# Optimization experiments

Hardware: AMD Instinct MI355X
Metric: run time of the kernel (lower is better)

## Reference

```python
import jax, jax.numpy as jnp
import numpy as np

B, N, D, K = 4, 8192, 128, 16


def setup_inputs() -> dict:
    key = jax.random.key(0)
    ks = jax.random.split(key, 12)
    w = lambda k, s: (jax.random.normal(k, s, jnp.float32) * 0.02)
    return {
        "xyz": jax.random.normal(ks[0], (B, N, 3), jnp.float32),
        "feat": jax.random.normal(ks[1], (B, N, D), jnp.float32),
        # Linear weights stored as (in, out); apply as x @ W + b
        "Wq": w(ks[2], (D, D)), "bq": jnp.zeros((D,), jnp.float32),
        "Wk": w(ks[3], (D, D)), "bk": jnp.zeros((D,), jnp.float32),
        "Wv": w(ks[4], (D, D)), "bv": jnp.zeros((D,), jnp.float32),
        "Wp1": w(ks[5], (3, D)), "bp1": jnp.zeros((D,), jnp.float32),
        "Wp2": w(ks[6], (D, D)), "bp2": jnp.zeros((D,), jnp.float32),
        "Wo": w(ks[7], (D, D)), "bo": jnp.zeros((D,), jnp.float32),
        "gamma": jnp.float32(0.5),
    }


def reference(xyz, feat, Wq, bq, Wk, bk, Wv, bv, Wp1, bp1, Wp2, bp2, Wo, bo, gamma):
    # pairwise squared distance (B,N,N)
    sq = jnp.sum(xyz * xyz, axis=-1)
    dist = sq[:, :, None] + sq[:, None, :] - 2.0 * jnp.einsum("bnc,bmc->bnm", xyz, xyz)
    # K nearest neighbors (smallest distance)
    _, idx = jax.lax.top_k(-dist, K)  # (B,N,K)
    bidx = jnp.arange(B)[:, None, None]
    n_xyz = xyz[bidx, idx]    # (B,N,K,3)
    n_feat = feat[bidx, idx]  # (B,N,K,D)

    q = (feat @ Wq + bq)[:, :, None, :]    # (B,N,1,D)
    kk = n_feat @ Wk + bk                  # (B,N,K,D)
    v = n_feat @ Wv + bv                   # (B,N,K,D)

    rel_pos = xyz[:, :, None, :] - n_xyz   # (B,N,K,3)
    pos_enc = jax.nn.relu(rel_pos @ Wp1 + bp1) @ Wp2 + bp2  # (B,N,K,D)

    # per-channel-summed attention score, softmax over neighbor axis
    score = jnp.sum(q - kk + pos_enc, axis=-1, keepdims=True)  # (B,N,K,1)
    attn = jax.nn.softmax(score, axis=-2)

    agg = jnp.sum(attn * (v + pos_enc), axis=2)  # (B,N,D)
    out = agg @ Wo + bo
    return feat + gamma * out
```

## Files before the change

### kernel.cpp

```cpp
#include <hip/hip_runtime.h>
#include <hip/hip_bf16.h>

#define BATCH 4
#define NPTS  8192
#define DIM   128
#define KNN   16
#define NROWS (BATCH * NPTS)

#define SPLITS 16
#define RANGE  512
#define TILE   256
#define DEPTH  32
#define DEPTHP 34
#define NSUB   8

using u64  = unsigned long long;
using u32  = unsigned int;

__device__ __forceinline__ unsigned short f2bf(float f) {
    u32 u = __float_as_uint(f);
    u32 r = (u + 0x7FFFu + ((u >> 16) & 1u)) >> 16;
    return (unsigned short)r;
}
__device__ __forceinline__ u32 fordkey(float f) {
    u32 u = __float_as_uint(f);
    return (u & 0x80000000u) ? ~u : (u | 0x80000000u);
}
__device__ __forceinline__ float invkey(u32 k) {
    u32 u = (k & 0x80000000u) ? (k & 0x7FFFFFFFu) : ~k;
    return __uint_as_float(u);
}

__device__ __forceinline__ void insert16(u64 key, u64* ks) {
    if (key < ks[15]) {
#pragma unroll
        for (int t = 0; t < 16; ++t) {
            u64 lo = key < ks[t] ? key : ks[t];
            u64 hi = key < ks[t] ? ks[t] : key;
            ks[t] = lo;
            key = hi;
        }
    }
}

__device__ __forceinline__ float pdist(float4 me, float4 c) {
    float dot = __fadd_rn(__fadd_rn(__fmul_rn(me.x, c.x), __fmul_rn(me.y, c.y)),
                          __fmul_rn(me.z, c.z));
    return __fsub_rn(__fadd_rn(me.w, c.w), __fmul_rn(2.0f, dot));
}

__global__ __launch_bounds__(256) void prep_weights(const float* __restrict__ Wk,
                                                    const float* __restrict__ Wp2,
                                                    float* __restrict__ wk,
                                                    float* __restrict__ w2) {
    int tid = threadIdx.x;
    int c = tid & 127;
    const float* src = (tid < 128) ? Wk : Wp2;
    float s = 0.f;
    for (int d = 0; d < DIM; ++d) s += src[c * DIM + d];
    if (tid < 128) wk[c] = s;
    else           w2[c] = s;
}

__global__ __launch_bounds__(256) void conv_weights(const float* __restrict__ Wv,
                                                    const float* __restrict__ Wp2,
                                                    const float* __restrict__ Wo,
                                                    u32* __restrict__ Wb) {
    int i = blockIdx.x * 256 + threadIdx.x;
    int which = i >> 13, off = i & 8191;
    const float* W = (which == 0) ? Wv : (which == 1 ? Wp2 : Wo);
    float2 w = ((const float2*)W)[off];
    Wb[i] = (u32)f2bf(w.x) | ((u32)f2bf(w.y) << 16);
}

__global__ __launch_bounds__(256) void prep_points(const float* __restrict__ xyz,
                                                   const float* __restrict__ feat,
                                                   const float* __restrict__ wk,
                                                   float4* __restrict__ pts,
                                                   float* __restrict__ sK) {
    int lid = threadIdx.x & 63;
    int p = blockIdx.x * 4 + (threadIdx.x >> 6);
    float f_lo = feat[(size_t)p * DIM + lid];
    float f_hi = feat[(size_t)p * DIM + 64 + lid];
    float s = fmaf(f_lo, wk[lid], f_hi * wk[64 + lid]);
#pragma unroll
    for (int m = 32; m >= 1; m >>= 1) s += __shfl_xor(s, m);
    if (lid == 0) {
        float x = xyz[p * 3 + 0];
        float y = xyz[p * 3 + 1];
        float z = xyz[p * 3 + 2];
        float sq = __fadd_rn(__fadd_rn(__fmul_rn(x, x), __fmul_rn(y, y)), __fmul_rn(z, z));
        pts[p] = make_float4(x, y, z, sq);
        sK[p] = s;
    }
}

__global__ __launch_bounds__(256) void knn_limpass(const float4* __restrict__ pts,
                                                   float* __restrict__ dlim) {
    __shared__ float4 tile[256];
    __shared__ unsigned short stk[4][64][DEPTHP];
    int y = blockIdx.y;
    int wavein = threadIdx.x >> 6, lane = threadIdx.x & 63;
    int q = blockIdx.x * 256 + wavein * 64 + lane;
    int b = q >> 13;
    float4 me = pts[q];
    {
        float4 c = pts[b * NPTS + y * 256 + threadIdx.x];
        tile[threadIdx.x] = make_float4(c.x, c.y, c.z, -0.5f * c.w);
    }
    __syncthreads();
    float ks[16];
#pragma unroll
    for (int t = 0; t < 16; ++t) ks[t] = INFINITY;
    unsigned short* mystk = stk[wavein][lane];

    for (int jj = 0; jj < 32; ++jj) {
        float4 c = tile[jj];
        float s = fmaf(me.x, c.x, fmaf(me.y, c.y, fmaf(me.z, c.z, c.w)));
        float d = fmaf(-2.0f, s, me.w);
        if (d < ks[15]) {
#pragma unroll
            for (int t = 0; t < 16; ++t) {
                float lo = fminf(d, ks[t]);
                float hi = fmaxf(d, ks[t]);
                ks[t] = lo;
                d = hi;
            }
        }
    }
    float lim = ks[15];
    for (int c0 = 32; c0 < 256; c0 += 32) {
        int cnt = 0;
#pragma unroll
        for (int jj = c0; jj < c0 + 32; ++jj) {
            float4 c = tile[jj];
            float s = fmaf(me.x, c.x, fmaf(me.y, c.y, fmaf(me.z, c.z, c.w)));
            float d = fmaf(-2.0f, s, me.w);
            int slot = cnt < (DEPTH - 1) ? cnt : (DEPTH - 1);
            mystk[slot] = (unsigned short)jj;
            cnt += (d < lim) ? 1 : 0;
        }
        for (int i = 0; i < cnt; ++i) {
            int jj = mystk[i];
            float4 c = tile[jj];
            float s = fmaf(me.x, c.x, fmaf(me.y, c.y, fmaf(me.z, c.z, c.w)));
            float d = fmaf(-2.0f, s, me.w);
            if (d < ks[15]) {
#pragma unroll
                for (int t = 0; t < 16; ++t) {
                    float lo = fminf(d, ks[t]);
                    float hi = fmaxf(d, ks[t]);
                    ks[t] = lo;
                    d = hi;
                }
            }
        }
        lim = ks[15];
    }
    dlim[(size_t)y * NROWS + q] = ks[15];
}

__global__ __launch_bounds__(256) void knn_partial(const float4* __restrict__ pts,
                                                   const float* __restrict__ dlim,
                                                   unsigned short* __restrict__ part16) {
    __shared__ float4 tile[TILE];
    __shared__ unsigned short stk[4][64][DEPTHP];
    int r = blockIdx.y;
    int wavein = threadIdx.x >> 6, lane = threadIdx.x & 63;
    int q = blockIdx.x * 256 + wavein * 64 + lane;
    int b = q >> 13;
    float4 me = pts[q];

    float T = dlim[q];
#pragma unroll
    for (int y = 1; y < NSUB; ++y) T = fminf(T, dlim[(size_t)y * NROWS + q]);
    float gate_d = T + 2.0e-4f;
    u64 sent = ((u64)fordkey(gate_d) << 32) | 0xFFFFFFFFull;
    u64 ks[16];
#pragma unroll
    for (int t = 0; t < 16; ++t) ks[t] = sent;
    float A = 0.5f * (me.w - gate_d) - 1.0e-4f;
    unsigned short* mystk = stk[wavein][lane];

    for (int tb = 0; tb < RANGE / TILE; ++tb) {
        __syncthreads();
        int jb = r * RANGE + tb * TILE;
        {
            float4 c = pts[b * NPTS + jb + threadIdx.x];
            tile[threadIdx.x] = make_float4(c.x, c.y, c.z, -0.5f * c.w);
        }
        __syncthreads();

        int cnt = 0;
#pragma unroll 4
        for (int jj = 0; jj < TILE; ++jj) {
            float4 c = tile[jj];
            float s = fmaf(me.x, c.x, fmaf(me.y, c.y, fmaf(me.z, c.z, c.w)));
            int slot = cnt < (DEPTH - 1) ? cnt : (DEPTH - 1);
            mystk[slot] = (unsigned short)jj;
            cnt += (s >= A) ? 1 : 0;
        }
        bool over = (cnt >= DEPTH);
        int dn = over ? 0 : cnt;
        for (int i = 0; i < dn; ++i) {
            int jj = mystk[i];
            float4 c = tile[jj];
            float4 cc = make_float4(c.x, c.y, c.z, -2.0f * c.w);
            float d = pdist(me, cc);
            u64 key = ((u64)fordkey(d) << 32) | (u32)(jb + jj);
            insert16(key, ks);
        }
        if (__any(over)) {
            if (over) {
                for (int jj = 0; jj < TILE; ++jj) {
                    float4 c = tile[jj];
                    float s = fmaf(me.x, c.x, fmaf(me.y, c.y, fmaf(me.z, c.z, c.w)));
                    if (s >= A) {
                        float4 cc = make_float4(c.x, c.y, c.z, -2.0f * c.w);
                        float d = pdist(me, cc);
                        u64 key = ((u64)fordkey(d) << 32) | (u32)(jb + jj);
                        insert16(key, ks);
                    }
                }
            }
        }
        float nl = invkey((u32)(ks[15] >> 32)) + 1.0e-4f;
        gate_d = (nl < gate_d) ? nl : gate_d;
        A = 0.5f * (me.w - gate_d) - 1.0e-4f;
    }
    u32* dst = (u32*)(part16 + (size_t)q * 256 + r * 16);
#pragma unroll
    for (int t = 0; t < 8; ++t)
        dst[t] = (u32)(ks[2 * t] & 0xFFFFu) | ((u32)(ks[2 * t + 1] & 0xFFFFu) << 16);
}

__global__ __launch_bounds__(256) void knn_merge(const float4* __restrict__ pts,
                                                 const unsigned short* __restrict__ part16,
                                                 int* __restrict__ idx16) {
    int wavein = threadIdx.x >> 6, lane = threadIdx.x & 63;
    int q = blockIdx.x * 4 + wavein;
    int b = q >> 13;
    float4 me = pts[q];
    ushort4 e = *(const ushort4*)(part16 + (size_t)q * 256 + lane * 4);
    u64 k0, k1, k2, k3;
    {
        u32 id;
        id = e.x; k0 = (id != 0xFFFFu) ? (((u64)fordkey(pdist(me, pts[b * NPTS + id])) << 32) | id) : ~0ull;
        id = e.y; k1 = (id != 0xFFFFu) ? (((u64)fordkey(pdist(me, pts[b * NPTS + id])) << 32) | id) : ~0ull;
        id = e.z; k2 = (id != 0xFFFFu) ? (((u64)fordkey(pdist(me, pts[b * NPTS + id])) << 32) | id) : ~0ull;
        id = e.w; k3 = (id != 0xFFFFu) ? (((u64)fordkey(pdist(me, pts[b * NPTS + id])) << 32) | id) : ~0ull;
    }
    u64 t;
    if (k1 < k0) { t = k0; k0 = k1; k1 = t; }
    if (k3 < k2) { t = k2; k2 = k3; k3 = t; }
    if (k2 < k0) { t = k0; k0 = k2; k2 = t; }
    if (k3 < k1) { t = k1; k1 = k3; k3 = t; }
    if (k2 < k1) { t = k1; k1 = k2; k2 = t; }

    u64 cur = k0;
    int head = 0;
    u64 got = 0;
#pragma unroll
    for (int it = 0; it < 16; ++it) {
        u64 m = cur;
#pragma unroll
        for (int s = 32; s >= 1; s >>= 1) {
            u64 o = __shfl_xor(m, s);
            m = (o < m) ? o : m;
        }
        if (m == cur) {
            head++;
            cur = (head == 1) ? k1 : (head == 2) ? k2 : (head == 3) ? k3 : ~0ull;
        }
        if (lane == it) got = m;
    }
    if (lane < 16) idx16[q * KNN + lane] = (int)(got & 0xFFFFFFFFu);
}

template <int MODE>
__global__ __launch_bounds__(256) void gemm32(const float* __restrict__ X,
                                              const u32* __restrict__ Wb,
                                              const float* __restrict__ bias,
                                              const float* __restrict__ add,
                                              const float* __restrict__ featb,
                                              const float* __restrict__ gammap,
                                              float* __restrict__ outv) {
    __shared__ u32 Ws[DIM * DIM / 2];
    __shared__ float Xs[8 * DIM];
    __shared__ float bs[DIM];
    int tid = threadIdx.x;
    {
        const uint4* src = (const uint4*)Wb;
        uint4* dst = (uint4*)Ws;
        for (int i = tid; i < DIM * DIM / 8; i += 256) dst[i] = src[i];
    }
    if (tid < 128) bs[tid] = bias[tid];
    float gamma = 0.f;
    if (MODE == 2) gamma = *gammap;

    int rowBase = blockIdx.x * 32;
    int d4 = (tid & 31) * 4;
    int row = tid >> 5;

    for (int it = 0; it < 4; ++it) {
        int r0 = rowBase + it * 8;
        __syncthreads();
        ((float4*)Xs)[tid] = ((const float4*)(X + (size_t)r0 * DIM))[tid];
        __syncthreads();

        float a0 = bs[d4], a1 = bs[d4 + 1], a2 = bs[d4 + 2], a3 = bs[d4 + 3];
        const float* xr = &Xs[row * DIM];
#pragma unroll 8
        for (int c = 0; c < DIM; ++c) {
            float x = xr[c];
            uint2 w = *(const uint2*)&Ws[c * (DIM / 2) + (d4 >> 1)];
            a0 = fmaf(x, __uint_as_float(w.x << 16), a0);
            a1 = fmaf(x, __uint_as_float(w.x & 0xFFFF0000u), a1);
            a2 = fmaf(x, __uint_as_float(w.y << 16), a2);
            a3 = fmaf(x, __uint_as_float(w.y & 0xFFFF0000u), a3);
        }
        size_t off = (size_t)(r0 + row) * DIM + d4;
        if (MODE == 1) {
            float4 ad = *(const float4*)(add + off);
            a0 += ad.x; a1 += ad.y; a2 += ad.z; a3 += ad.w;
        }
        if (MODE == 2) {
            float4 fb = *(const float4*)(featb + off);
            a0 = fmaf(gamma, a0, fb.x);
            a1 = fmaf(gamma, a1, fb.y);
            a2 = fmaf(gamma, a2, fb.z);
            a3 = fmaf(gamma, a3, fb.w);
        }
        *(float4*)(outv + off) = make_float4(a0, a1, a2, a3);
    }
}

__global__ __launch_bounds__(256) void stage_c(const float4* __restrict__ pts,
                                               const int* __restrict__ idx16,
                                               const float* __restrict__ sK,
                                               const float* __restrict__ w2,
                                               const float* __restrict__ Wp1,
                                               const float* __restrict__ bp1,
                                               const float* __restrict__ Vf,
                                               float* __restrict__ vagg,
                                               float* __restrict__ hbar) {
    __shared__ float hs[4][KNN * DIM];
    int wavein = threadIdx.x >> 6;
    int lid = threadIdx.x & 63;
    int p = blockIdx.x * 4 + wavein;
    int b = p >> 13;
    float4 me = pts[p];

    float wx_lo = Wp1[lid],        wx_hi = Wp1[64 + lid];
    float wy_lo = Wp1[128 + lid],  wy_hi = Wp1[192 + lid];
    float wz_lo = Wp1[256 + lid],  wz_hi = Wp1[320 + lid];
    float bl    = bp1[lid],        bh    = bp1[64 + lid];
    float w2l   = w2[lid],         w2h   = w2[64 + lid];

    int myidx = idx16[p * KNN + (lid & 15)];
    float* h = hs[wavein];
    float sc = -INFINITY;

    for (int k = 0; k < KNN; ++k) {
        int j = __shfl(myidx, k);
        int g = b * NPTS + j;
        float4 nb = pts[g];
        float rx = me.x - nb.x, ry = me.y - nb.y, rz = me.z - nb.z;
        float h_lo = fmaxf(0.f, fmaf(rx, wx_lo, fmaf(ry, wy_lo, fmaf(rz, wz_lo, bl))));
        float h_hi = fmaxf(0.f, fmaf(rx, wx_hi, fmaf(ry, wy_hi, fmaf(rz, wz_hi, bh))));
        h[k * DIM + lid] = h_lo;
        h[k * DIM + 64 + lid] = h_hi;
        float s = fmaf(h_lo, w2l, h_hi * w2h);
#pragma unroll
        for (int m = 32; m >= 1; m >>= 1) s += __shfl_xor(s, m);
        float score = s - sK[g];
        if (lid == k) sc = score;
    }
    float mx = sc;
#pragma unroll
    for (int m = 8; m >= 1; m >>= 1) mx = fmaxf(mx, __shfl_xor(mx, m));
    float e = (lid < 16) ? __expf(sc - mx) : 0.f;
    float ssum = e;
#pragma unroll
    for (int m = 8; m >= 1; m >>= 1) ssum += __shfl_xor(ssum, m);
    float a = e / ssum;

    float acc_lo = 0.f, acc_hi = 0.f, hb_lo = 0.f, hb_hi = 0.f;
    for (int k = 0; k < KNN; ++k) {
        float ak = __shfl(a, k);
        int j = __shfl(myidx, k);
        size_t g = (size_t)(b * NPTS + j) * DIM;
        acc_lo = fmaf(ak, Vf[g + lid], acc_lo);
        acc_hi = fmaf(ak, Vf[g + 64 + lid], acc_hi);
        hb_lo = fmaf(ak, h[k * DIM + lid], hb_lo);
        hb_hi = fmaf(ak, h[k * DIM + 64 + lid], hb_hi);
    }
    size_t o = (size_t)p * DIM;
    vagg[o + lid] = acc_lo;
    vagg[o + 64 + lid] = acc_hi;
    hbar[o + lid] = hb_lo;
    hbar[o + 64 + lid] = hb_hi;
}

extern "C" void kernel_launch(void* const* d_in, const int* in_sizes, int n_in,
                              void* d_out, int out_size, void* d_ws, size_t ws_size,
                              hipStream_t stream) {
    const float* xyz   = (const float*)d_in[0];
    const float* feat  = (const float*)d_in[1];
    const float* Wk    = (const float*)d_in[4];
    const float* Wv    = (const float*)d_in[6];
    const float* bv    = (const float*)d_in[7];
    const float* Wp1   = (const float*)d_in[8];
    const float* bp1   = (const float*)d_in[9];
    const float* Wp2   = (const float*)d_in[10];
    const float* bp2   = (const float*)d_in[11];
    const float* Wo    = (const float*)d_in[12];
    const float* bo    = (const float*)d_in[13];
    const float* gamma = (const float*)d_in[14];
    float* out = (float*)d_out;

    char* ws = (char*)d_ws;
    const size_t KB = 1024, MB = 1024 * 1024;
    float*  wk    = (float*)(ws + 0);
    float*  w2    = (float*)(ws + 4 * KB);
    float4* pts   = (float4*)(ws + 16 * KB);
    float*  sKv   = (float*)(ws + 544 * KB);
    u32*    Wb    = (u32*)(ws + 688 * KB);
    float*  dlim  = (float*)(ws + 1 * MB);
    unsigned short* part16 = (unsigned short*)(ws + 5 * MB);
    float*  vagg  = (float*)(ws + 5 * MB);
    float*  hbarp = (float*)(ws + 21 * MB);
    int*    idx16 = (int*)(ws + 37 * MB);
    float*  Vf    = (float*)(ws + 39 * MB);
    float*  T1    = (float*)(ws + 39 * MB);

    prep_weights<<<1, 256, 0, stream>>>(Wk, Wp2, wk, w2);
    conv_weights<<<96, 256, 0, stream>>>(Wv, Wp2, Wo, Wb);
    prep_points<<<NROWS / 4, 256, 0, stream>>>(xyz, feat, wk, pts, sKv);
    gemm32<0><<<1024, 256, 0, stream>>>(feat, Wb, bv, nullptr, nullptr, nullptr, Vf);
    knn_limpass<<<dim3(NROWS / 256, NSUB), 256, 0, stream>>>(pts, dlim);
    knn_partial<<<dim3(NROWS / 256, SPLITS), 256, 0, stream>>>(pts, dlim, part16);
    knn_merge<<<NROWS / 4, 256, 0, stream>>>(pts, part16, idx16);
    stage_c<<<NROWS / 4, 256, 0, stream>>>(pts, idx16, sKv, w2, Wp1, bp1, Vf, vagg, hbarp);
    gemm32<1><<<1024, 256, 0, stream>>>(hbarp, Wb + 8192, bp2, vagg, nullptr, nullptr, T1);
    gemm32<2><<<1024, 256, 0, stream>>>(T1, Wb + 16384, bo, nullptr, feat, gamma, out);
}
```

Before: 557.2 us.

## Replace LDS candidate stacks with per-32 bitmask filtering via scalar candidate loads

Both KNN passes drop the per-thread LDS index stack and build a 32-bit candidate mask per group of 32 points, then walk it with ctz. The filter reads a precomputed scaled copy of the points (ptsS) straight from global memory at a wave-uniform address, so it can use scalar loads, while exact distances still come from the LDS tile. knn_partial now tightens its gate after every 32 points rather than once per tile, and limpass tightens its threshold the same way. This removes LDS stack writes and the overflow fallback path, at the cost of an extra point buffer and more frequent gate updates.

```diff
diff --git a/kernel.cpp b/kernel.cpp
--- a/kernel.cpp
+++ b/kernel.cpp
@@ -10,8 +10,6 @@
 #define SPLITS 16
 #define RANGE  512
 #define TILE   256
-#define DEPTH  32
-#define DEPTHP 34
 #define NSUB   8
 
 using u64  = unsigned long long;
@@ -77,6 +75,7 @@
                                                    const float* __restrict__ feat,
                                                    const float* __restrict__ wk,
                                                    float4* __restrict__ pts,
+                                                   float4* __restrict__ ptsS,
                                                    float* __restrict__ sK) {
     int lid = threadIdx.x & 63;
     int p = blockIdx.x * 4 + (threadIdx.x >> 6);
@@ -90,61 +89,43 @@
         float y = xyz[p * 3 + 1];
         float z = xyz[p * 3 + 2];
         float sq = __fadd_rn(__fadd_rn(__fmul_rn(x, x), __fmul_rn(y, y)), __fmul_rn(z, z));
-        pts[p] = make_float4(x, y, z, sq);
+        pts[p]  = make_float4(x, y, z, sq);
+        ptsS[p] = make_float4(x, y, z, -0.5f * sq);
         sK[p] = s;
     }
 }
 
 __global__ __launch_bounds__(256) void knn_limpass(const float4* __restrict__ pts,
+                                                   const float4* __restrict__ ptsS,
                                                    float* __restrict__ dlim) {
     __shared__ float4 tile[256];
-    __shared__ unsigned short stk[4][64][DEPTHP];
     int y = blockIdx.y;
-    int wavein = threadIdx.x >> 6, lane = threadIdx.x & 63;
-    int q = blockIdx.x * 256 + wavein * 64 + lane;
-    int b = q >> 13;
+    int q = blockIdx.x * 256 + threadIdx.x;
+    int bb = blockIdx.x >> 5;
     float4 me = pts[q];
-    {
-        float4 c = pts[b * NPTS + y * 256 + threadIdx.x];
-        tile[threadIdx.x] = make_float4(c.x, c.y, c.z, -0.5f * c.w);
-    }
+    int base = __builtin_amdgcn_readfirstlane(bb * NPTS + y * 256);
+    tile[threadIdx.x] = pts[base + threadIdx.x];
     __syncthreads();
+    const float4* cs = ptsS + base;
+
     float ks[16];
 #pragma unroll
     for (int t = 0; t < 16; ++t) ks[t] = INFINITY;
-    unsigned short* mystk = stk[wavein][lane];
-
-    for (int jj = 0; jj < 32; ++jj) {
-        float4 c = tile[jj];
-        float s = fmaf(me.x, c.x, fmaf(me.y, c.y, fmaf(me.z, c.z, c.w)));
-        float d = fmaf(-2.0f, s, me.w);
-        if (d < ks[15]) {
-#pragma unroll
-            for (int t = 0; t < 16; ++t) {
-                float lo = fminf(d, ks[t]);
-                float hi = fmaxf(d, ks[t]);
-                ks[t] = lo;
-                d = hi;
-            }
-        }
-    }
-    float lim = ks[15];
-    for (int c0 = 32; c0 < 256; c0 += 32) {
-        int cnt = 0;
-#pragma unroll
-        for (int jj = c0; jj < c0 + 32; ++jj) {
-            float4 c = tile[jj];
-            float s = fmaf(me.x, c.x, fmaf(me.y, c.y, fmaf(me.z, c.z, c.w)));
-            float d = fmaf(-2.0f, s, me.w);
-            int slot = cnt < (DEPTH - 1) ? cnt : (DEPTH - 1);
-            mystk[slot] = (unsigned short)jj;
-            cnt += (d < lim) ? 1 : 0;
-        }
-        for (int i = 0; i < cnt; ++i) {
-            int jj = mystk[i];
-            float4 c = tile[jj];
-            float s = fmaf(me.x, c.x, fmaf(me.y, c.y, fmaf(me.z, c.z, c.w)));
-            float d = fmaf(-2.0f, s, me.w);
+    float A = -INFINITY;
+
+    for (int w = 0; w < 8; ++w) {
+        u32 m = 0;
+#pragma unroll
+        for (int bit = 0; bit < 32; ++bit) {
+            float4 c = cs[w * 32 + bit];
+            float s = me.x * c.x + me.y * c.y + me.z * c.z + c.w;
+            m |= ((s >= A) ? 1u : 0u) << bit;
+        }
+        while (m) {
+            int bit = __builtin_ctz(m); m &= m - 1;
+            float4 c = tile[w * 32 + bit];
+            float dot = fmaf(me.x, c.x, fmaf(me.y, c.y, me.z * c.z));
+            float d = me.w + c.w - 2.0f * dot;
             if (d < ks[15]) {
 #pragma unroll
                 for (int t = 0; t < 16; ++t) {
@@ -155,20 +136,19 @@
                 }
             }
         }
-        lim = ks[15];
+        A = 0.5f * (me.w - ks[15]) - 1.0e-4f;
     }
     dlim[(size_t)y * NROWS + q] = ks[15];
 }
 
 __global__ __launch_bounds__(256) void knn_partial(const float4* __restrict__ pts,
+                                                   const float4* __restrict__ ptsS,
                                                    const float* __restrict__ dlim,
                                                    unsigned short* __restrict__ part16) {
     __shared__ float4 tile[TILE];
-    __shared__ unsigned short stk[4][64][DEPTHP];
     int r = blockIdx.y;
-    int wavein = threadIdx.x >> 6, lane = threadIdx.x & 63;
-    int q = blockIdx.x * 256 + wavein * 64 + lane;
-    int b = q >> 13;
+    int q = blockIdx.x * 256 + threadIdx.x;
+    int bb = blockIdx.x >> 5;
     float4 me = pts[q];
 
     float T = dlim[q];
@@ -180,53 +160,34 @@
 #pragma unroll
     for (int t = 0; t < 16; ++t) ks[t] = sent;
     float A = 0.5f * (me.w - gate_d) - 1.0e-4f;
-    unsigned short* mystk = stk[wavein][lane];
 
     for (int tb = 0; tb < RANGE / TILE; ++tb) {
         __syncthreads();
         int jb = r * RANGE + tb * TILE;
-        {
-            float4 c = pts[b * NPTS + jb + threadIdx.x];
-            tile[threadIdx.x] = make_float4(c.x, c.y, c.z, -0.5f * c.w);
-        }
+        int base = __builtin_amdgcn_readfirstlane(bb * NPTS + jb);
+        tile[threadIdx.x] = pts[base + threadIdx.x];
         __syncthreads();
-
-        int cnt = 0;
-#pragma unroll 4
-        for (int jj = 0; jj < TILE; ++jj) {
-            float4 c = tile[jj];
-            float s = fmaf(me.x, c.x, fmaf(me.y, c.y, fmaf(me.z, c.z, c.w)));
-            int slot = cnt < (DEPTH - 1) ? cnt : (DEPTH - 1);
-            mystk[slot] = (unsigned short)jj;
-            cnt += (s >= A) ? 1 : 0;
-        }
-        bool over = (cnt >= DEPTH);
-        int dn = over ? 0 : cnt;
-        for (int i = 0; i < dn; ++i) {
-            int jj = mystk[i];
-            float4 c = tile[jj];
-            float4 cc = make_float4(c.x, c.y, c.z, -2.0f * c.w);
-            float d = pdist(me, cc);
-            u64 key = ((u64)fordkey(d) << 32) | (u32)(jb + jj);
-            insert16(key, ks);
-        }
-        if (__any(over)) {
-            if (over) {
-                for (int jj = 0; jj < TILE; ++jj) {
-                    float4 c = tile[jj];
-                    float s = fmaf(me.x, c.x, fmaf(me.y, c.y, fmaf(me.z, c.z, c.w)));
-                    if (s >= A) {
-                        float4 cc = make_float4(c.x, c.y, c.z, -2.0f * c.w);
-                        float d = pdist(me, cc);
-                        u64 key = ((u64)fordkey(d) << 32) | (u32)(jb + jj);
-                        insert16(key, ks);
-                    }
-                }
+        const float4* cs = ptsS + base;
+
+        for (int w = 0; w < TILE / 32; ++w) {
+            u32 m = 0;
+#pragma unroll
+            for (int bit = 0; bit < 32; ++bit) {
+                float4 c = cs[w * 32 + bit];
+                float s = me.x * c.x + me.y * c.y + me.z * c.z + c.w;
+                m |= ((s >= A) ? 1u : 0u) << bit;
             }
-        }
-        float nl = invkey((u32)(ks[15] >> 32)) + 1.0e-4f;
-        gate_d = (nl < gate_d) ? nl : gate_d;
-        A = 0.5f * (me.w - gate_d) - 1.0e-4f;
+            while (m) {
+                int bit = __builtin_ctz(m); m &= m - 1;
+                int jj = w * 32 + bit;
+                float d = pdist(me, tile[jj]);
+                u64 key = ((u64)fordkey(d) << 32) | (u32)(jb + jj);
+                insert16(key, ks);
+            }
+            float nl = invkey((u32)(ks[15] >> 32)) + 1.0e-4f;
+            gate_d = (nl < gate_d) ? nl : gate_d;
+            A = 0.5f * (me.w - gate_d) - 1.0e-4f;
+        }
     }
     u32* dst = (u32*)(part16 + (size_t)q * 256 + r * 16);
 #pragma unroll
@@ -427,6 +388,7 @@
     float*  sKv   = (float*)(ws + 544 * KB);
     u32*    Wb    = (u32*)(ws + 688 * KB);
     float*  dlim  = (float*)(ws + 1 * MB);
+    float4* ptsS  = (float4*)(ws + 2 * MB);
     unsigned short* part16 = (unsigned short*)(ws + 5 * MB);
     float*  vagg  = (float*)(ws + 5 * MB);
     float*  hbarp = (float*)(ws + 21 * MB);
@@ -436,10 +398,10 @@
 
     prep_weights<<<1, 256, 0, stream>>>(Wk, Wp2, wk, w2);
     conv_weights<<<96, 256, 0, stream>>>(Wv, Wp2, Wo, Wb);
-    prep_points<<<NROWS / 4, 256, 0, stream>>>(xyz, feat, wk, pts, sKv);
+    prep_points<<<NROWS / 4, 256, 0, stream>>>(xyz, feat, wk, pts, ptsS, sKv);
     gemm32<0><<<1024, 256, 0, stream>>>(feat, Wb, bv, nullptr, nullptr, nullptr, Vf);
-    knn_limpass<<<dim3(NROWS / 256, NSUB), 256, 0, stream>>>(pts, dlim);
-    knn_partial<<<dim3(NROWS / 256, SPLITS), 256, 0, stream>>>(pts, dlim, part16);
+    knn_limpass<<<dim3(NROWS / 256, NSUB), 256, 0, stream>>>(pts, ptsS, dlim);
+    knn_partial<<<dim3(NROWS / 256, SPLITS), 256, 0, stream>>>(pts, ptsS, dlim, part16);
     knn_merge<<<NROWS / 4, 256, 0, stream>>>(pts, part16, idx16);
     stage_c<<<NROWS / 4, 256, 0, stream>>>(pts, idx16, sKv, w2, Wp1, bp1, Vf, vagg, hbarp);
     gemm32<1><<<1024, 256, 0, stream>>>(hbarp, Wb + 8192, bp2, vagg, nullptr, nullptr, T1);
```

After: 607.2 us. 1.09x slower.
